# Kernel tuning notes

Measured on AMD Instinct MI355X. Metric: run time of the kernel, lower is better.

## Reference

```python
import jax, jax.numpy as jnp
import numpy as np
import math

HEADS = 12

def setup_inputs() -> dict:
    key = jax.random.key(0)
    ks = jax.random.split(key, 5)
    E = 768
    r, i, n = 64, 256, 2
    s = 0.02  # init scale for weights
    return {
        "x": jax.random.normal(ks[0], (r, i, n, E), dtype=jnp.float32),
        "Wq": jax.random.normal(ks[1], (E, E), dtype=jnp.float32) * s,
        "bq": jnp.zeros((E,), dtype=jnp.float32),
        "Wk": jax.random.normal(ks[2], (E, E), dtype=jnp.float32) * s,
        "bk": jnp.zeros((E,), dtype=jnp.float32),
        "Wv": jax.random.normal(ks[3], (E, E), dtype=jnp.float32) * s,
        "bv": jnp.zeros((E,), dtype=jnp.float32),
        "Wo": jax.random.normal(ks[4], (E, E), dtype=jnp.float32) * s,
        "bo": jnp.zeros((E,), dtype=jnp.float32),
    }


def reference(x, Wq, bq, Wk, bk, Wv, bv, Wo, bo):
    r, i, n, E = x.shape
    h = HEADS
    d = E // h
    shape = (r, i, n, h, d)
    q = (x @ Wq + bq).reshape(shape)
    k = (x @ Wk + bk).reshape(shape)
    v = (x @ Wv + bv).reshape(shape)
    # tied row attention: 1/sqrt(d) softmax scale plus 1/sqrt(num_rows) for row sum
    scaling = d ** (-0.5) / math.sqrt(r)
    q = q * scaling
    # scores shared across all rows: contract over row axis r and head dim d
    attn_weights = jnp.einsum('rinhd,rjnhd->hnij', q, k)  # [h, n, i, j]
    attn_probs = jax.nn.softmax(attn_weights, axis=-1)
    # dropout disabled (deterministic=True)
    context = jnp.einsum('hnij,rjnhd->rinhd', attn_probs, v)
    context = context.reshape(r, i, n, E)
    return context @ Wo + bo
```

## Files before the change

### kernel.cpp

```cpp
#include <hip/hip_runtime.h>
#include <stdint.h>

typedef __attribute__((ext_vector_type(8))) short bf16x8;
typedef __attribute__((ext_vector_type(4))) float f32x4;
typedef __attribute__((ext_vector_type(4))) unsigned short us4;
typedef __attribute__((ext_vector_type(8))) unsigned short us8;

static __device__ __forceinline__ unsigned short f2bf(float f) {
  union { float f; unsigned u; } c; c.f = f;
  unsigned r = c.u + 0x7fffu + ((c.u >> 16) & 1u);
  return (unsigned short)(r >> 16);
}

static __device__ __forceinline__ void gl_lds16(const unsigned short* g, unsigned short* l) {
  __builtin_amdgcn_global_load_lds(
      (const __attribute__((address_space(1))) unsigned int*)g,
      (__attribute__((address_space(3))) unsigned int*)l, 16, 0, 0);
}

#define LDP 80

#define QT 16384

__device__ __forceinline__ void gemm256_core(
    const unsigned short* __restrict__ Ag, int lda,
    const unsigned short* __restrict__ Bg, int ldb,
    int K, unsigned short* As, unsigned short* Bs, f32x4 acc[8][4])
{
  const int tid  = threadIdx.x;
  const int lane = tid & 63;
  const int wid  = tid >> 6;
  const int wr = wid >> 2, wc = wid & 3;
  const int lr = lane & 15, kg = lane >> 4;
  const int l7 = lane & 7;
  const int srow = tid >> 3;
  const int sch  = (tid & 7) ^ (srow & 7);

  auto STG = [&](int c, int kt, int bufo) {
    int row = c * 64 + srow;
    gl_lds16(Ag + row * lda + kt + sch * 8, As + bufo + ((c * 512 + wid * 64) << 3));
    gl_lds16(Bg + row * ldb + kt + sch * 8, Bs + bufo + ((c * 512 + wid * 64) << 3));
  };

  const int nt = K >> 6;
  STG(0, 0, 0); STG(1, 0, 0); STG(2, 0, 0); STG(3, 0, 0);
  int cur = 0;
  for (int t = 0; t < nt; ++t) {
    const bool last = (t == nt - 1);
    const int kt1 = (t + 1) << 6;
    const int cb = cur * QT, nb = (cur ^ 1) * QT;
    if (!last) STG(0, kt1, nb);
    if (last) asm volatile("s_waitcnt vmcnt(0)" ::: "memory");
    else      asm volatile("s_waitcnt vmcnt(2)" ::: "memory");
    __builtin_amdgcn_s_barrier();
    bf16x8 bf[4][2];
#pragma unroll
    for (int ni = 0; ni < 4; ++ni)
#pragma unroll
      for (int ks = 0; ks < 2; ++ks)
        bf[ni][ks] = *reinterpret_cast<const bf16x8*>(
            Bs + cb + (wc*64 + ni*16 + lr) * 64 + (((ks*4 + kg) ^ l7) << 3));
#pragma unroll
    for (int q = 0; q < 4; ++q) {
      bf16x8 af[2][2];
#pragma unroll
      for (int m2 = 0; m2 < 2; ++m2)
#pragma unroll
        for (int ks = 0; ks < 2; ++ks)
          af[m2][ks] = *reinterpret_cast<const bf16x8*>(
              As + cb + (wr*128 + (q*2 + m2)*16 + lr) * 64 + (((ks*4 + kg) ^ l7) << 3));
      if (!last && q < 3) STG(q + 1, kt1, nb);
      __builtin_amdgcn_s_setprio(1);
#pragma unroll
      for (int ks = 0; ks < 2; ++ks)
#pragma unroll
        for (int m2 = 0; m2 < 2; ++m2)
#pragma unroll
          for (int ni = 0; ni < 4; ++ni)
            acc[q*2 + m2][ni] = __builtin_amdgcn_mfma_f32_16x16x32_bf16(
                af[m2][ks], bf[ni][ks], acc[q*2 + m2][ni], 0, 0, 0);
      __builtin_amdgcn_s_setprio(0);
    }
    __builtin_amdgcn_s_barrier();
    cur ^= 1;
  }
}

__device__ __forceinline__ void stage8(
    const unsigned short* __restrict__ Ag, int lda,
    const unsigned short* __restrict__ Bg, int ldb, int kt,
    unsigned short* As, unsigned short* Bs, int tid, int wid)
{
#pragma unroll
  for (int c = 0; c < 4; ++c) {
    int chunk = c * 256 + tid;
    int row = chunk >> 3, u = chunk & 7;
    int ch = u ^ (row & 7);
    gl_lds16(Ag + row * lda + kt + ch * 8, As + ((c * 256 + wid * 64) << 3));
    gl_lds16(Bg + row * ldb + kt + ch * 8, Bs + ((c * 256 + wid * 64) << 3));
  }
}

__device__ __forceinline__ void compute64(
    const unsigned short* As, const unsigned short* Bs, f32x4 acc[4][4],
    int wr, int wc, int lr, int kg, int l7)
{
#pragma unroll
  for (int ks = 0; ks < 2; ++ks) {
    bf16x8 af[4], bfr[4];
    int u = (ks * 4 + kg) ^ l7;
#pragma unroll
    for (int mi = 0; mi < 4; ++mi)
      af[mi] = *reinterpret_cast<const bf16x8*>(As + (wr*64 + mi*16 + lr) * 64 + u * 8);
#pragma unroll
    for (int ni = 0; ni < 4; ++ni)
      bfr[ni] = *reinterpret_cast<const bf16x8*>(Bs + (wc*64 + ni*16 + lr) * 64 + u * 8);
#pragma unroll
    for (int mi = 0; mi < 4; ++mi)
#pragma unroll
      for (int ni = 0; ni < 4; ++ni)
        acc[mi][ni] = __builtin_amdgcn_mfma_f32_16x16x32_bf16(af[mi], bfr[ni], acc[mi][ni], 0, 0, 0);
  }
}

__device__ __forceinline__ void gemm_core(
    const unsigned short* __restrict__ Ag, int lda,
    const unsigned short* __restrict__ Bg, int ldb,
    int K, unsigned short* As, unsigned short* Bs, f32x4 acc[4][4])
{
  const int tid  = threadIdx.x;
  const int lane = tid & 63;
  const int wid  = tid >> 6;
  const int wr = wid >> 1, wc = wid & 1;
  const int lr = lane & 15, kg = lane >> 4;
  const int l7 = lane & 7;

  const int nt = K >> 6;
  stage8(Ag, lda, Bg, ldb, 0, As, Bs, tid, wid);
  int cur = 0;
  for (int t = 0; t < nt - 1; ++t) {
    stage8(Ag, lda, Bg, ldb, (t + 1) << 6,
           As + (cur ^ 1) * 8192, Bs + (cur ^ 1) * 8192, tid, wid);
    asm volatile("s_waitcnt vmcnt(8)" ::: "memory");
    __builtin_amdgcn_s_barrier();
    compute64(As + cur * 8192, Bs + cur * 8192, acc, wr, wc, lr, kg, l7);
    __builtin_amdgcn_s_barrier();
    cur ^= 1;
  }
  asm volatile("s_waitcnt vmcnt(0)" ::: "memory");
  __builtin_amdgcn_s_barrier();
  compute64(As + cur * 8192, Bs + cur * 8192, acc, wr, wc, lr, kg, l7);
}

#define ACC_ZERO(acc) do { \
  f32x4 z = {0.f, 0.f, 0.f, 0.f}; \
  for (int a_ = 0; a_ < 4; ++a_) for (int b_ = 0; b_ < 4; ++b_) acc[a_][b_] = z; } while (0)

#define ACC_ZERO8(acc) do { \
  f32x4 z = {0.f, 0.f, 0.f, 0.f}; \
  for (int a_ = 0; a_ < 8; ++a_) for (int b_ = 0; b_ < 4; ++b_) acc[a_][b_] = z; } while (0)

#define EPI_VARS \
  int tid = threadIdx.x, lane = tid & 63, wid = tid >> 6; \
  int wr = wid >> 1, wc = wid & 1, lr = lane & 15, kg = lane >> 4; (void)wr; (void)wc;

#define GEMM_LDS \
  __shared__ unsigned short As[2 * 128 * 64], Bs[2 * 128 * 64];


__global__ __launch_bounds__(256) void k_cvt_x(const float* __restrict__ x,
                                               unsigned short* __restrict__ xb) {
  int i = blockIdx.x * 256 + threadIdx.x;
  f32x4 f = reinterpret_cast<const f32x4*>(x)[i];
  us4 o = { f2bf(f[0]), f2bf(f[1]), f2bf(f[2]), f2bf(f[3]) };
  reinterpret_cast<us4*>(xb)[i] = o;
}

__global__ __launch_bounds__(256) void k_cvt_w(
    const float* __restrict__ Wq, const float* __restrict__ Wk, const float* __restrict__ Wv,
    const float* __restrict__ Wo, const float* __restrict__ bq, const float* __restrict__ bk,
    const float* __restrict__ bv, unsigned short* __restrict__ wT,
    unsigned short* __restrict__ woT, float* __restrict__ bqkv)
{
  const float qs = 1.0f / 64.0f;
  int o = blockIdx.x * 256 + threadIdx.x;
  if (o < 2304 * 768) {
    int col = o / 768, k = o % 768;
    float v;
    if (col < 768)       v = Wq[k * 768 + col] * qs;
    else if (col < 1536) v = Wk[k * 768 + col - 768];
    else                 v = Wv[k * 768 + col - 1536];
    wT[o] = f2bf(v);
  } else if (o < 2304 * 768 + 768 * 768) {
    int o2 = o - 2304 * 768;
    int col = o2 / 768, k = o2 % 768;
    woT[o2] = f2bf(Wo[k * 768 + col]);
  } else {
    int o3 = o - (2304 * 768 + 768 * 768);
    float v = (o3 < 768) ? bq[o3] * qs : (o3 < 1536 ? bk[o3 - 768] : bv[o3 - 1536]);
    bqkv[o3] = v;
  }
}

__global__ __launch_bounds__(512, 2) void k_gemm_qkv(
    const unsigned short* __restrict__ xb, const unsigned short* __restrict__ wT,
    const float* __restrict__ bqkv, unsigned short* __restrict__ qkvb)
{
  __shared__ unsigned short As[2 * QT], Bs[2 * QT];
  int bx = blockIdx.x, bn = bx % 9, bm = bx / 9;
  f32x4 acc[8][4]; ACC_ZERO8(acc);
  gemm256_core(xb + (size_t)bm * 256 * 768, 768, wT + (size_t)bn * 256 * 768, 768,
               768, As, Bs, acc);
  const int lane = threadIdx.x & 63, wid = threadIdx.x >> 6;
  const int wr = wid >> 2, wc = wid & 3, lr = lane & 15, kg = lane >> 4;
#pragma unroll
  for (int mi = 0; mi < 8; ++mi)
#pragma unroll
    for (int ni = 0; ni < 4; ++ni) {
      int col = bn * 256 + wc * 64 + ni * 16 + lr;
      float bias = bqkv[col];
#pragma unroll
      for (int e = 0; e < 4; ++e) {
        int row = bm * 256 + wr * 128 + mi * 16 + kg * 4 + e;
        qkvb[(size_t)row * 2304 + col] = f2bf(acc[mi][ni][e] + bias);
      }
    }
}

__global__ __launch_bounds__(256) void k_repack_v(
    const unsigned short* __restrict__ qkvb, unsigned short* __restrict__ V)
{
  __shared__ unsigned short lds[64 * LDP];
  int bx = blockIdx.x;
  int jt = bx & 3, rr = (bx >> 2) & 63, hn = bx >> 8;
  int h = hn >> 1, nn = hn & 1;
  int t = threadIdx.x;
  int j = t >> 3, ch = t & 7;
#pragma unroll
  for (int p = 0; p < 2; ++p) {
    int jj = p * 32 + j;
    us8 v = *reinterpret_cast<const us8*>(
        qkvb + ((size_t)((rr * 256 + jt * 64 + jj) * 2 + nn)) * 2304 + 1536 + h * 64 + ch * 8);
#pragma unroll
    for (int e = 0; e < 8; ++e) lds[(ch * 8 + e) * LDP + jj] = v[e];
  }
  __syncthreads();
  int dd = t >> 2, cj = t & 3;
  size_t ob = ((size_t)(hn * 64 + rr) * 64) * 256;
#pragma unroll
  for (int p = 0; p < 2; ++p) {
    int c2 = cj + p * 4;
    us8 v = *reinterpret_cast<const us8*>(lds + dd * LDP + c2 * 8);
    *reinterpret_cast<us8*>(V + ob + (size_t)dd * 256 + jt * 64 + c2 * 8) = v;
  }
}

__global__ __launch_bounds__(256) void k_gemm_scores(
    const unsigned short* __restrict__ qkvb, float* __restrict__ Spart)
{
  __shared__ unsigned short Asp[128 * LDP], Bsp[128 * LDP];
  int bx = blockIdx.x;
  int s = bx / 96, rblk = bx % 96;
  int hn = rblk >> 2, tt = rblk & 3, bm = tt >> 1, bn = tt & 1;
  int h = hn >> 1, nn = hn & 1;
  const int hq = h * 64;
  f32x4 acc[4][4]; ACC_ZERO(acc);

  const int tid = threadIdx.x, lane = tid & 63, wid = tid >> 6;
  const int wr = wid >> 1, wc = wid & 1, lr = lane & 15, kg = lane >> 4;
  const int srow = tid >> 3, sch = tid & 7;

  for (int t = 0; t < 16; ++t) {
    int rr = s * 16 + t;
    us8 av[4], bv[4];
#pragma unroll
    for (int c = 0; c < 4; ++c) {
      int row = c * 32 + srow;
      size_t ab = ((size_t)((rr * 256 + bm * 128 + row) * 2 + nn)) * 2304 + hq + sch * 8;
      size_t bb = ((size_t)((rr * 256 + bn * 128 + row) * 2 + nn)) * 2304 + 768 + hq + sch * 8;
      av[c] = *reinterpret_cast<const us8*>(qkvb + ab);
      bv[c] = *reinterpret_cast<const us8*>(qkvb + bb);
    }
    __syncthreads();
#pragma unroll
    for (int c = 0; c < 4; ++c) {
      int row = c * 32 + srow;
      *reinterpret_cast<us8*>(Asp + row * LDP + sch * 8) = av[c];
      *reinterpret_cast<us8*>(Bsp + row * LDP + sch * 8) = bv[c];
    }
    __syncthreads();
#pragma unroll
    for (int ks = 0; ks < 2; ++ks) {
      bf16x8 af[4], bfr[4];
#pragma unroll
      for (int mi = 0; mi < 4; ++mi)
        af[mi] = *reinterpret_cast<const bf16x8*>(Asp + (wr*64 + mi*16 + lr) * LDP + ks*32 + kg*8);
#pragma unroll
      for (int ni = 0; ni < 4; ++ni)
        bfr[ni] = *reinterpret_cast<const bf16x8*>(Bsp + (wc*64 + ni*16 + lr) * LDP + ks*32 + kg*8);
#pragma unroll
      for (int mi = 0; mi < 4; ++mi)
#pragma unroll
        for (int ni = 0; ni < 4; ++ni)
          acc[mi][ni] = __builtin_amdgcn_mfma_f32_16x16x32_bf16(af[mi], bfr[ni], acc[mi][ni], 0, 0, 0);
    }
  }

  float* Ss = Spart + ((size_t)s * 24 + hn) * 65536;
#pragma unroll
  for (int mi = 0; mi < 4; ++mi)
#pragma unroll
    for (int ni = 0; ni < 4; ++ni)
#pragma unroll
      for (int e = 0; e < 4; ++e) {
        int row = bm * 128 + wr * 64 + mi * 16 + kg * 4 + e;
        int col = bn * 128 + wc * 64 + ni * 16 + lr;
        Ss[(size_t)row * 256 + col] = acc[mi][ni][e];
      }
}

__global__ __launch_bounds__(256) void k_softmax(const float* __restrict__ Sp,
                                                 unsigned short* __restrict__ P)
{
  __shared__ float red[8];
  size_t row = blockIdx.x;
  int t = threadIdx.x, wid = t >> 6, lane = t & 63;
  size_t idx = row * 256 + t;
  float v = Sp[idx] + Sp[idx + 1572864] + Sp[idx + 2 * 1572864] + Sp[idx + 3 * 1572864];
  float m = v;
#pragma unroll
  for (int o = 32; o; o >>= 1) m = fmaxf(m, __shfl_xor(m, o));
  if (lane == 0) red[wid] = m;
  __syncthreads();
  m = fmaxf(fmaxf(red[0], red[1]), fmaxf(red[2], red[3]));
  float e = __expf(v - m);
  float sm = e;
#pragma unroll
  for (int o = 32; o; o >>= 1) sm += __shfl_xor(sm, o);
  if (lane == 0) red[4 + wid] = sm;
  __syncthreads();
  sm = red[4] + red[5] + red[6] + red[7];
  P[row * 256 + t] = f2bf(e / sm);
}

__global__ __launch_bounds__(256) void k_gemm_ctx(
    const unsigned short* __restrict__ P, const unsigned short* __restrict__ V,
    unsigned short* __restrict__ Cb)
{
  GEMM_LDS;
  int bx = blockIdx.x;
  int hn = bx / 64, tt = bx % 64, bm = tt >> 5, bn = tt & 31;
  f32x4 acc[4][4]; ACC_ZERO(acc);
  const unsigned short* Ag = P + (size_t)hn * 65536 + (size_t)bm * 128 * 256;
  const unsigned short* Bg = V + (size_t)hn * 4096 * 256 + (size_t)bn * 128 * 256;
  gemm_core(Ag, 256, Bg, 256, 256, As, Bs, acc);
  EPI_VARS;
  int nn = hn & 1;
  int h = hn >> 1;
#pragma unroll
  for (int mi = 0; mi < 4; ++mi)
#pragma unroll
    for (int ni = 0; ni < 4; ++ni) {
      int c = bn * 128 + wc * 64 + ni * 16 + lr;
      int rr = c >> 6, dd = c & 63;
#pragma unroll
      for (int e = 0; e < 4; ++e) {
        int i = bm * 128 + wr * 64 + mi * 16 + kg * 4 + e;
        int tok = (rr * 256 + i) * 2 + nn;
        Cb[(size_t)tok * 768 + h * 64 + dd] = f2bf(acc[mi][ni][e]);
      }
    }
}

__global__ __launch_bounds__(512, 2) void k_gemm_out(
    const unsigned short* __restrict__ Cb, const unsigned short* __restrict__ woT,
    const float* __restrict__ bo, float* __restrict__ out)
{
  __shared__ unsigned short As[2 * QT], Bs[2 * QT];
  int bx = blockIdx.x, bn = bx % 3, bm = bx / 3;
  f32x4 acc[8][4]; ACC_ZERO8(acc);
  gemm256_core(Cb + (size_t)bm * 256 * 768, 768, woT + (size_t)bn * 256 * 768, 768,
               768, As, Bs, acc);
  const int lane = threadIdx.x & 63, wid = threadIdx.x >> 6;
  const int wr = wid >> 2, wc = wid & 3, lr = lane & 15, kg = lane >> 4;
#pragma unroll
  for (int mi = 0; mi < 8; ++mi)
#pragma unroll
    for (int ni = 0; ni < 4; ++ni) {
      int col = bn * 256 + wc * 64 + ni * 16 + lr;
      float bias = bo[col];
#pragma unroll
      for (int e = 0; e < 4; ++e) {
        int row = bm * 256 + wr * 128 + mi * 16 + kg * 4 + e;
        out[(size_t)row * 768 + col] = acc[mi][ni][e] + bias;
      }
    }
}

extern "C" void kernel_launch(void* const* d_in, const int* in_sizes, int n_in,
                              void* d_out, int out_size, void* d_ws, size_t ws_size,
                              hipStream_t stream)
{
  const float* x  = (const float*)d_in[0];
  const float* Wq = (const float*)d_in[1];
  const float* bq = (const float*)d_in[2];
  const float* Wk = (const float*)d_in[3];
  const float* bk = (const float*)d_in[4];
  const float* Wv = (const float*)d_in[5];
  const float* bv = (const float*)d_in[6];
  const float* Wo = (const float*)d_in[7];
  const float* bo = (const float*)d_in[8];
  float* out = (float*)d_out;

  char* ws = (char*)d_ws;
  size_t off = 0;
  auto alloc = [&](size_t bytes) { void* p = ws + off; off += (bytes + 255) & ~(size_t)255; return p; };
  unsigned short* xb   = (unsigned short*)alloc(50331648);
  unsigned short* qkvb = (unsigned short*)alloc(150994944);
  unsigned short* Vb   = (unsigned short*)alloc(50331648);
  unsigned short* Cb   = (unsigned short*)alloc(50331648);
  unsigned short* wT   = (unsigned short*)alloc(3538944);
  unsigned short* woT  = (unsigned short*)alloc(1179648);
  float*          bqkv = (float*)alloc(9216);
  if (off > ws_size) return;

  float*          Sp = (float*)d_out;
  unsigned short* P  = (unsigned short*)((char*)d_out + 25165824);

  k_cvt_x      <<<24576, 256, 0, stream>>>(x, xb);
  k_cvt_w      <<<9225,  256, 0, stream>>>(Wq, Wk, Wv, Wo, bq, bk, bv, wT, woT, bqkv);
  k_gemm_qkv   <<<1152,  512, 0, stream>>>(xb, wT, bqkv, qkvb);
  k_repack_v   <<<6144,  256, 0, stream>>>(qkvb, Vb);
  k_gemm_scores<<<384,   256, 0, stream>>>(qkvb, Sp);
  k_softmax    <<<6144,  256, 0, stream>>>(Sp, P);
  k_gemm_ctx   <<<1536,  256, 0, stream>>>(P, Vb, Cb);
  k_gemm_out   <<<384,   512, 0, stream>>>(Cb, woT, bo, out);
}
```

Measured before the change: 366.5 us.

## Merge conversion and scores/repack launches, retile output GEMM to 128x128

```diff
diff --git a/kernel.cpp b/kernel.cpp
--- a/kernel.cpp
+++ b/kernel.cpp
@@ -19,7 +19,6 @@
 }
 
 #define LDP 80
-
 #define QT 16384
 
 __device__ __forceinline__ void gemm256_core(
@@ -168,22 +167,23 @@
   __shared__ unsigned short As[2 * 128 * 64], Bs[2 * 128 * 64];
 
 
-__global__ __launch_bounds__(256) void k_cvt_x(const float* __restrict__ x,
-                                               unsigned short* __restrict__ xb) {
-  int i = blockIdx.x * 256 + threadIdx.x;
-  f32x4 f = reinterpret_cast<const f32x4*>(x)[i];
-  us4 o = { f2bf(f[0]), f2bf(f[1]), f2bf(f[2]), f2bf(f[3]) };
-  reinterpret_cast<us4*>(xb)[i] = o;
-}
-
-__global__ __launch_bounds__(256) void k_cvt_w(
+__global__ __launch_bounds__(256) void k_cvt_xw(
+    const float* __restrict__ x, unsigned short* __restrict__ xb,
     const float* __restrict__ Wq, const float* __restrict__ Wk, const float* __restrict__ Wv,
     const float* __restrict__ Wo, const float* __restrict__ bq, const float* __restrict__ bk,
     const float* __restrict__ bv, unsigned short* __restrict__ wT,
     unsigned short* __restrict__ woT, float* __restrict__ bqkv)
 {
+  int b = blockIdx.x;
+  if (b < 24576) {
+    int i = b * 256 + threadIdx.x;
+    f32x4 f = reinterpret_cast<const f32x4*>(x)[i];
+    us4 o = { f2bf(f[0]), f2bf(f[1]), f2bf(f[2]), f2bf(f[3]) };
+    reinterpret_cast<us4*>(xb)[i] = o;
+    return;
+  }
   const float qs = 1.0f / 64.0f;
-  int o = blockIdx.x * 256 + threadIdx.x;
+  int o = (b - 24576) * 256 + threadIdx.x;
   if (o < 2304 * 768) {
     int col = o / 768, k = o % 768;
     float v;
@@ -227,11 +227,75 @@
     }
 }
 
-__global__ __launch_bounds__(256) void k_repack_v(
-    const unsigned short* __restrict__ qkvb, unsigned short* __restrict__ V)
-{
-  __shared__ unsigned short lds[64 * LDP];
-  int bx = blockIdx.x;
+__global__ __launch_bounds__(256) void k_scores_repack(
+    const unsigned short* __restrict__ qkvb, float* __restrict__ Spart,
+    unsigned short* __restrict__ V)
+{
+  __shared__ unsigned short Asp[128 * LDP], Bsp[128 * LDP];
+  int b = blockIdx.x;
+  if (b < 384) {
+    int s = b / 96, rblk = b % 96;
+    int hn = rblk >> 2, tt = rblk & 3, bm = tt >> 1, bn = tt & 1;
+    int h = hn >> 1, nn = hn & 1;
+    const int hq = h * 64;
+    f32x4 acc[4][4]; ACC_ZERO(acc);
+
+    const int tid = threadIdx.x, lane = tid & 63, wid = tid >> 6;
+    const int wr = wid >> 1, wc = wid & 1, lr = lane & 15, kg = lane >> 4;
+    const int srow = tid >> 3, sch = tid & 7;
+
+    for (int t = 0; t < 16; ++t) {
+      int rr = s * 16 + t;
+      us8 av[4], bv[4];
+#pragma unroll
+      for (int c = 0; c < 4; ++c) {
+        int row = c * 32 + srow;
+        size_t ab = ((size_t)((rr * 256 + bm * 128 + row) * 2 + nn)) * 2304 + hq + sch * 8;
+        size_t bb = ((size_t)((rr * 256 + bn * 128 + row) * 2 + nn)) * 2304 + 768 + hq + sch * 8;
+        av[c] = *reinterpret_cast<const us8*>(qkvb + ab);
+        bv[c] = *reinterpret_cast<const us8*>(qkvb + bb);
+      }
+      __syncthreads();
+#pragma unroll
+      for (int c = 0; c < 4; ++c) {
+        int row = c * 32 + srow;
+        *reinterpret_cast<us8*>(Asp + row * LDP + sch * 8) = av[c];
+        *reinterpret_cast<us8*>(Bsp + row * LDP + sch * 8) = bv[c];
+      }
+      __syncthreads();
+#pragma unroll
+      for (int ks = 0; ks < 2; ++ks) {
+        bf16x8 af[4], bfr[4];
+#pragma unroll
+        for (int mi = 0; mi < 4; ++mi)
+          af[mi] = *reinterpret_cast<const bf16x8*>(Asp + (wr*64 + mi*16 + lr) * LDP + ks*32 + kg*8);
+#pragma unroll
+        for (int ni = 0; ni < 4; ++ni)
+          bfr[ni] = *reinterpret_cast<const bf16x8*>(Bsp + (wc*64 + ni*16 + lr) * LDP + ks*32 + kg*8);
+#pragma unroll
+        for (int mi = 0; mi < 4; ++mi)
+#pragma unroll
+          for (int ni = 0; ni < 4; ++ni)
+            acc[mi][ni] = __builtin_amdgcn_mfma_f32_16x16x32_bf16(af[mi], bfr[ni], acc[mi][ni], 0, 0, 0);
+      }
+    }
+
+    float* Ss = Spart + ((size_t)s * 24 + hn) * 65536;
+#pragma unroll
+    for (int mi = 0; mi < 4; ++mi)
+#pragma unroll
+      for (int ni = 0; ni < 4; ++ni)
+#pragma unroll
+        for (int e = 0; e < 4; ++e) {
+          int row = bm * 128 + wr * 64 + mi * 16 + kg * 4 + e;
+          int col = bn * 128 + wc * 64 + ni * 16 + lr;
+          Ss[(size_t)row * 256 + col] = acc[mi][ni][e];
+        }
+    return;
+  }
+
+  unsigned short* lds = Asp;
+  int bx = b - 384;
   int jt = bx & 3, rr = (bx >> 2) & 63, hn = bx >> 8;
   int h = hn >> 1, nn = hn & 1;
   int t = threadIdx.x;
@@ -253,70 +317,6 @@
     us8 v = *reinterpret_cast<const us8*>(lds + dd * LDP + c2 * 8);
     *reinterpret_cast<us8*>(V + ob + (size_t)dd * 256 + jt * 64 + c2 * 8) = v;
   }
-}
-
-__global__ __launch_bounds__(256) void k_gemm_scores(
-    const unsigned short* __restrict__ qkvb, float* __restrict__ Spart)
-{
-  __shared__ unsigned short Asp[128 * LDP], Bsp[128 * LDP];
-  int bx = blockIdx.x;
-  int s = bx / 96, rblk = bx % 96;
-  int hn = rblk >> 2, tt = rblk & 3, bm = tt >> 1, bn = tt & 1;
-  int h = hn >> 1, nn = hn & 1;
-  const int hq = h * 64;
-  f32x4 acc[4][4]; ACC_ZERO(acc);
-
-  const int tid = threadIdx.x, lane = tid & 63, wid = tid >> 6;
-  const int wr = wid >> 1, wc = wid & 1, lr = lane & 15, kg = lane >> 4;
-  const int srow = tid >> 3, sch = tid & 7;
-
-  for (int t = 0; t < 16; ++t) {
-    int rr = s * 16 + t;
-    us8 av[4], bv[4];
-#pragma unroll
-    for (int c = 0; c < 4; ++c) {
-      int row = c * 32 + srow;
-      size_t ab = ((size_t)((rr * 256 + bm * 128 + row) * 2 + nn)) * 2304 + hq + sch * 8;
-      size_t bb = ((size_t)((rr * 256 + bn * 128 + row) * 2 + nn)) * 2304 + 768 + hq + sch * 8;
-      av[c] = *reinterpret_cast<const us8*>(qkvb + ab);
-      bv[c] = *reinterpret_cast<const us8*>(qkvb + bb);
-    }
-    __syncthreads();
-#pragma unroll
-    for (int c = 0; c < 4; ++c) {
-      int row = c * 32 + srow;
-      *reinterpret_cast<us8*>(Asp + row * LDP + sch * 8) = av[c];
-      *reinterpret_cast<us8*>(Bsp + row * LDP + sch * 8) = bv[c];
-    }
-    __syncthreads();
-#pragma unroll
-    for (int ks = 0; ks < 2; ++ks) {
-      bf16x8 af[4], bfr[4];
-#pragma unroll
-      for (int mi = 0; mi < 4; ++mi)
-        af[mi] = *reinterpret_cast<const bf16x8*>(Asp + (wr*64 + mi*16 + lr) * LDP + ks*32 + kg*8);
-#pragma unroll
-      for (int ni = 0; ni < 4; ++ni)
-        bfr[ni] = *reinterpret_cast<const bf16x8*>(Bsp + (wc*64 + ni*16 + lr) * LDP + ks*32 + kg*8);
-#pragma unroll
-      for (int mi = 0; mi < 4; ++mi)
-#pragma unroll
-        for (int ni = 0; ni < 4; ++ni)
-          acc[mi][ni] = __builtin_amdgcn_mfma_f32_16x16x32_bf16(af[mi], bfr[ni], acc[mi][ni], 0, 0, 0);
-    }
-  }
-
-  float* Ss = Spart + ((size_t)s * 24 + hn) * 65536;
-#pragma unroll
-  for (int mi = 0; mi < 4; ++mi)
-#pragma unroll
-    for (int ni = 0; ni < 4; ++ni)
-#pragma unroll
-      for (int e = 0; e < 4; ++e) {
-        int row = bm * 128 + wr * 64 + mi * 16 + kg * 4 + e;
-        int col = bn * 128 + wc * 64 + ni * 16 + lr;
-        Ss[(size_t)row * 256 + col] = acc[mi][ni][e];
-      }
 }
 
 __global__ __launch_bounds__(256) void k_softmax(const float* __restrict__ Sp,
@@ -372,26 +372,26 @@
     }
 }
 
-__global__ __launch_bounds__(512, 2) void k_gemm_out(
+__global__ __launch_bounds__(256) void k_gemm_out(
     const unsigned short* __restrict__ Cb, const unsigned short* __restrict__ woT,
     const float* __restrict__ bo, float* __restrict__ out)
 {
-  __shared__ unsigned short As[2 * QT], Bs[2 * QT];
-  int bx = blockIdx.x, bn = bx % 3, bm = bx / 3;
-  f32x4 acc[8][4]; ACC_ZERO8(acc);
-  gemm256_core(Cb + (size_t)bm * 256 * 768, 768, woT + (size_t)bn * 256 * 768, 768,
-               768, As, Bs, acc);
-  const int lane = threadIdx.x & 63, wid = threadIdx.x >> 6;
-  const int wr = wid >> 2, wc = wid & 3, lr = lane & 15, kg = lane >> 4;
-#pragma unroll
-  for (int mi = 0; mi < 8; ++mi)
+  GEMM_LDS;
+  int b0 = blockIdx.x;
+  int bx = (b0 & 7) * 192 + (b0 >> 3);
+  int bn = bx % 6, bm = bx / 6;
+  f32x4 acc[4][4]; ACC_ZERO(acc);
+  gemm_core(Cb + (size_t)bm * 128 * 768, 768, woT + (size_t)bn * 128 * 768, 768, 768, As, Bs, acc);
+  EPI_VARS;
+#pragma unroll
+  for (int mi = 0; mi < 4; ++mi)
 #pragma unroll
     for (int ni = 0; ni < 4; ++ni) {
-      int col = bn * 256 + wc * 64 + ni * 16 + lr;
+      int col = bn * 128 + wc * 64 + ni * 16 + lr;
       float bias = bo[col];
 #pragma unroll
       for (int e = 0; e < 4; ++e) {
-        int row = bm * 256 + wr * 128 + mi * 16 + kg * 4 + e;
+        int row = bm * 128 + wr * 64 + mi * 16 + kg * 4 + e;
         out[(size_t)row * 768 + col] = acc[mi][ni][e] + bias;
       }
     }
@@ -427,12 +427,10 @@
   float*          Sp = (float*)d_out;
   unsigned short* P  = (unsigned short*)((char*)d_out + 25165824);
 
-  k_cvt_x      <<<24576, 256, 0, stream>>>(x, xb);
-  k_cvt_w      <<<9225,  256, 0, stream>>>(Wq, Wk, Wv, Wo, bq, bk, bv, wT, woT, bqkv);
-  k_gemm_qkv   <<<1152,  512, 0, stream>>>(xb, wT, bqkv, qkvb);
-  k_repack_v   <<<6144,  256, 0, stream>>>(qkvb, Vb);
-  k_gemm_scores<<<384,   256, 0, stream>>>(qkvb, Sp);
-  k_softmax    <<<6144,  256, 0, stream>>>(Sp, P);
-  k_gemm_ctx   <<<1536,  256, 0, stream>>>(P, Vb, Cb);
-  k_gemm_out   <<<384,   512, 0, stream>>>(Cb, woT, bo, out);
-}
+  k_cvt_xw       <<<33801, 256, 0, stream>>>(x, xb, Wq, Wk, Wv, Wo, bq, bk, bv, wT, woT, bqkv);
+  k_gemm_qkv     <<<1152,  512, 0, stream>>>(xb, wT, bqkv, qkvb);
+  k_scores_repack<<<6528,  256, 0, stream>>>(qkvb, Sp, Vb);
+  k_softmax      <<<6144,  256, 0, stream>>>(Sp, P);
+  k_gemm_ctx     <<<1536,  256, 0, stream>>>(P, Vb, Cb);
+  k_gemm_out     <<<1536,  256, 0, stream>>>(Cb, woT, bo, out);
+}
```

Measured after the change: 336.6 us, median of 2. 8.1% less time.
